# Kernel tuning notes

Hardware: AMD Instinct MI355X
Metric: run time of the kernel (lower is better)

Reference implementation:

```python
import jax, jax.numpy as jnp
import numpy as np

NU, NF, E, FIN, H = 50000, 25000, 500000, 128, 128
NEG_SLOPE_ATT = 0.2   # PyG GATConv default negative_slope
NEG_SLOPE_MLP = 0.01  # nn.LeakyReLU default
BN_EPS = 1e-5


def setup_inputs() -> dict:
    key = jax.random.key(0)
    ks = iter(jax.random.split(key, 64))

    def rn(shape, scale=0.05):
        return jax.random.normal(next(ks), shape, dtype=jnp.float32) * scale

    inp = {
        "x_user": jax.random.normal(next(ks), (NU, FIN), dtype=jnp.float32),
        "x_food": jax.random.normal(next(ks), (NF, FIN), dtype=jnp.float32),
        "uf_src": jax.random.randint(next(ks), (E,), 0, NU),
        "uf_dst": jax.random.randint(next(ks), (E,), 0, NF),
        "fu_src": jax.random.randint(next(ks), (E,), 0, NF),
        "fu_dst": jax.random.randint(next(ks), (E,), 0, NU),
        "he_user": jax.random.randint(next(ks), (E,), 0, NU),
        "he_food": jax.random.randint(next(ks), (E,), 0, NF),
        "batch_health_scores": jax.random.uniform(next(ks), (E,), dtype=jnp.float32),
    }
    # GATConv params per layer (1,2) per edge type (uf: user->food, fu: food->user)
    for L, fin in ((1, FIN), (2, H)):
        for et in ("uf", "fu"):
            inp[f"w{L}_{et}_src"] = rn((fin, H))
            inp[f"w{L}_{et}_dst"] = rn((fin, H))
            inp[f"a{L}_{et}_src"] = rn((H,))
            inp[f"a{L}_{et}_dst"] = rn((H,))
            inp[f"b{L}_{et}"] = jnp.zeros((H,), jnp.float32)
    # BatchNorm per layer per node type
    for L in (1, 2):
        for nt in ("user", "food"):
            inp[f"bn{L}_{nt}_g"] = jnp.ones((H,), jnp.float32)
            inp[f"bn{L}_{nt}_b"] = jnp.zeros((H,), jnp.float32)
    # health preference MLP: Linear(H, H//2) -> LeakyReLU -> Linear(H//2, 1) -> Tanh
    inp["hw1"] = rn((H, H // 2)); inp["hb1"] = jnp.zeros((H // 2,), jnp.float32)
    inp["hw2"] = rn((H // 2, 1)); inp["hb2"] = jnp.zeros((1,), jnp.float32)
    return inp


def _gat(x_src, x_dst, src, dst, w_s, w_d, a_s, a_d, b, n_dst):
    """PyG GATConv, heads=1, no self loops, eval (no attention dropout)."""
    hs = x_src @ w_s                      # [Ns, H]
    hd = x_dst @ w_d                      # [Nd, H]
    asn = hs @ a_s                        # per-src-node scalar
    adn = hd @ a_d                        # per-dst-node scalar
    e = jax.nn.leaky_relu(asn[src] + adn[dst], NEG_SLOPE_ATT)  # [E]
    m = jax.ops.segment_max(e, dst, num_segments=n_dst)
    m = jnp.where(jnp.isfinite(m), m, 0.0)
    ee = jnp.exp(e - m[dst])
    den = jax.ops.segment_sum(ee, dst, num_segments=n_dst)
    alpha = ee / (den[dst] + 1e-16)
    out = jax.ops.segment_sum(alpha[:, None] * hs[src], dst, num_segments=n_dst)
    return out + b


def _bn_elu(x, g, b):
    mu = x.mean(0)
    var = x.var(0)  # biased var, as torch BN uses for normalization
    return jax.nn.elu((x - mu) * jax.lax.rsqrt(var + BN_EPS) * g + b)


def reference(x_user, x_food, uf_src, uf_dst, fu_src, fu_dst, he_user, he_food,
              batch_health_scores,
              w1_uf_src, w1_uf_dst, a1_uf_src, a1_uf_dst, b1_uf,
              w1_fu_src, w1_fu_dst, a1_fu_src, a1_fu_dst, b1_fu,
              w2_uf_src, w2_uf_dst, a2_uf_src, a2_uf_dst, b2_uf,
              w2_fu_src, w2_fu_dst, a2_fu_src, a2_fu_dst, b2_fu,
              bn1_user_g, bn1_user_b, bn1_food_g, bn1_food_b,
              bn2_user_g, bn2_user_b, bn2_food_g, bn2_food_b,
              hw1, hb1, hw2, hb2):
    # ---- layer 1 (HeteroConv, sum aggr; each node type has one incoming edge type)
    xf = _gat(x_user, x_food, uf_src, uf_dst, w1_uf_src, w1_uf_dst, a1_uf_src, a1_uf_dst, b1_uf, NF)
    xu = _gat(x_food, x_user, fu_src, fu_dst, w1_fu_src, w1_fu_dst, a1_fu_src, a1_fu_dst, b1_fu, NU)
    xu = _bn_elu(xu, bn1_user_g, bn1_user_b)
    xf = _bn_elu(xf, bn1_food_g, bn1_food_b)
    # ---- layer 2
    xf2 = _gat(xu, xf, uf_src, uf_dst, w2_uf_src, w2_uf_dst, a2_uf_src, a2_uf_dst, b2_uf, NF)
    xu2 = _gat(xf, xu, fu_src, fu_dst, w2_fu_src, w2_fu_dst, a2_fu_src, a2_fu_dst, b2_fu, NU)
    xu2 = _bn_elu(xu2, bn2_user_g, bn2_user_b)
    xf2 = _bn_elu(xf2, bn2_food_g, bn2_food_b)
    # ---- health-score scatter_add update
    h = jax.nn.leaky_relu(xu2 @ hw1 + hb1, NEG_SLOPE_MLP)
    prefs = jnp.tanh(h @ hw2 + hb2)                      # [NU, 1]
    adjusted = prefs[he_user, 0] * batch_health_scores   # [E]
    # expand+scatter_add over rows == broadcast segment_sum of the per-edge scalar
    s = jax.ops.segment_sum(adjusted, he_food, num_segments=NF)  # [NF]
    xf2 = xf2 + 0.1 * s[:, None]
    return (xu2, xf2, prefs)
```

## Files before the change

kernel.cpp:

```cpp
#include <hip/hip_runtime.h>
#include <cstddef>

#define NU_ 50000
#define NF_ 25000
#define E_  500000
#define CAPF_ 96
#define CAPU_ 48

typedef __attribute__((ext_vector_type(8))) short short8v;
typedef __attribute__((ext_vector_type(4))) float float4v;

constexpr int LDR = 136;

static __device__ __forceinline__ ushort f2bf(float f) {
    uint u = __float_as_uint(f);
    uint r = (u + 0x7fffu + ((u >> 16) & 1u)) >> 16;
    return (ushort)r;
}
static __device__ __forceinline__ float bf2f(ushort u) {
    return __uint_as_float(((uint)u) << 16);
}

struct PPArgs {
    const int* uf_src; const int* uf_dst;
    const int* fu_src; const int* fu_dst;
    int* deg_f; int* deg_u;
    int* buck_f; int* buck_u;
    const float* xu; const float* xf;
    ushort* bu; ushort* bfo;
    const float* W[5];  ushort* T[5];
    const float* waW[8]; const float* waA[8];
    float* vall;
};

__global__ __launch_bounds__(256) void preprocess(PPArgs A) {
    const int EB  = (E_ + 255) / 256;
    const int nbA = NU_ * 32 / 256;
    const int nbB = NF_ * 32 / 256;
    const int nbC = 4 * 64 + 32;
    int b = blockIdx.x, t = threadIdx.x;
    if (b < 2 * EB) {
        const int *src, *dst; int *deg, *buck; int cap, e;
        if (b < EB) { src = A.uf_src; dst = A.uf_dst; deg = A.deg_f; buck = A.buck_f; cap = CAPF_; e = b * 256 + t; }
        else        { src = A.fu_src; dst = A.fu_dst; deg = A.deg_u; buck = A.buck_u; cap = CAPU_; e = (b - EB) * 256 + t; }
        if (e < E_) {
            int d = dst[e];
            int r = atomicAdd(&deg[d], 1);
            if (r < cap) buck[d * cap + r] = src[e];
        }
        return;
    }
    b -= 2 * EB;
    if (b < nbA) {
        int i = b * 256 + t;
        float4 v = ((const float4*)A.xu)[i];
        ushort4 o; o.x = f2bf(v.x); o.y = f2bf(v.y); o.z = f2bf(v.z); o.w = f2bf(v.w);
        ((ushort4*)A.bu)[i] = o;
    } else if (b < nbA + nbB) {
        int i = (b - nbA) * 256 + t;
        float4 v = ((const float4*)A.xf)[i];
        ushort4 o; o.x = f2bf(v.x); o.y = f2bf(v.y); o.z = f2bf(v.z); o.w = f2bf(v.w);
        ((ushort4*)A.bfo)[i] = o;
    } else if (b < nbA + nbB + nbC) {
        int cb = b - nbA - nbB;
        int m, wb, sh;
        if (cb < 256) { m = cb >> 6; wb = cb & 63; sh = 7; }
        else          { m = 4; wb = cb - 256; sh = 6; }
        int idx = wb * 256 + t;
        int k = idx >> sh, c = idx & ((1 << sh) - 1);
        A.T[m][c * 128 + k] = f2bf(A.W[m][idx]);
    } else {
        int db = b - nbA - nbB - nbC;
        int row = db * 4 + (t >> 6);
        int m = row >> 7, k = row & 127, lane = t & 63;
        float2 w = ((const float2*)(A.waW[m] + k * 128))[lane];
        float2 av = ((const float2*)A.waA[m])[lane];
        float s = w.x * av.x + w.y * av.y;
        #pragma unroll
        for (int o = 32; o; o >>= 1) s += __shfl_xor(s, o);
        if (lane == 0) A.vall[row] = s;
    }
}

static __device__ __forceinline__ void gemm_tile(const ushort* __restrict__ Xb,
                                                 const ushort* __restrict__ Wt,
                                                 ushort* __restrict__ C, int N, int row0,
                                                 short* Xs, short* Ws) {
    const int t = threadIdx.x;
    for (int i = t; i < 128 * 16; i += 256) {
        int r = i >> 4, c8 = (i & 15) << 3;
        short8v v = {};
        if (row0 + r < N) v = *(const short8v*)(Xb + (size_t)(row0 + r) * 128 + c8);
        *(short8v*)(&Xs[r * LDR + c8]) = v;
    }
    for (int i = t; i < 128 * 16; i += 256) {
        int r = i >> 4, c8 = (i & 15) << 3;
        *(short8v*)(&Ws[r * LDR + c8]) = *(const short8v*)(Wt + r * 128 + c8);
    }
    __syncthreads();

    const int w = t >> 6, l = t & 63;
    const int m0 = (w & 1) * 64;
    const int n0 = (w >> 1) * 64;
    const int frow = l & 15;
    const int koff = (l >> 4) << 3;

    float4v acc[4][4];
    #pragma unroll
    for (int m = 0; m < 4; ++m)
        #pragma unroll
        for (int n = 0; n < 4; ++n) acc[m][n] = (float4v)0.f;

    #pragma unroll
    for (int ks = 0; ks < 4; ++ks) {
        const int k0 = ks * 32 + koff;
        short8v a[4], b[4];
        #pragma unroll
        for (int m = 0; m < 4; ++m)
            a[m] = *(const short8v*)(&Xs[(m0 + m * 16 + frow) * LDR + k0]);
        #pragma unroll
        for (int n = 0; n < 4; ++n)
            b[n] = *(const short8v*)(&Ws[(n0 + n * 16 + frow) * LDR + k0]);
        #pragma unroll
        for (int m = 0; m < 4; ++m)
            #pragma unroll
            for (int n = 0; n < 4; ++n)
                acc[m][n] = __builtin_amdgcn_mfma_f32_16x16x32_bf16(a[m], b[n], acc[m][n], 0, 0, 0);
    }

    const int crow = (l >> 4) << 2;
    const int ccol = l & 15;
    #pragma unroll
    for (int m = 0; m < 4; ++m) {
        #pragma unroll
        for (int r4 = 0; r4 < 4; ++r4) {
            int grow = row0 + m0 + m * 16 + crow + r4;
            if (grow < N) {
                #pragma unroll
                for (int n = 0; n < 4; ++n)
                    C[(size_t)grow * 128 + n0 + n * 16 + ccol] = f2bf(acc[m][n][r4]);
            }
        }
    }
}

__global__ __launch_bounds__(256) void gemm_both(const ushort* __restrict__ Xu, const ushort* __restrict__ Wtu,
                                                 ushort* __restrict__ Cu,
                                                 const ushort* __restrict__ Xf, const ushort* __restrict__ Wtf,
                                                 ushort* __restrict__ Cf) {
    __shared__ short Xs[128 * LDR];
    __shared__ short Ws[128 * LDR];
    const int GU = (NU_ + 127) / 128;
    if ((int)blockIdx.x < GU)
        gemm_tile(Xu, Wtu, Cu, NU_, blockIdx.x * 128, Xs, Ws);
    else
        gemm_tile(Xf, Wtf, Cf, NF_, (blockIdx.x - GU) * 128, Xs, Ws);
}

__global__ __launch_bounds__(256) void matvec4(const ushort* __restrict__ bu, const ushort* __restrict__ bfo,
                                               const float* __restrict__ v_asn_u, const float* __restrict__ v_adn_u,
                                               const float* __restrict__ v_adn_f, const float* __restrict__ v_asn_f,
                                               float* __restrict__ asn_u, float* __restrict__ adn_u,
                                               float* __restrict__ adn_f, float* __restrict__ asn_f) {
    int row = blockIdx.x * 4 + (threadIdx.x >> 6);
    int lane = threadIdx.x & 63;
    const ushort* X; const float *va, *vb; float *oa, *ob; int r;
    if (row < NU_) { X = bu; va = v_asn_u; vb = v_adn_u; oa = asn_u; ob = adn_u; r = row; }
    else {
        r = row - NU_;
        if (r >= NF_) return;
        X = bfo; va = v_adn_f; vb = v_asn_f; oa = adn_f; ob = asn_f;
    }
    ushort2 x = ((const ushort2*)(X + (size_t)r * 128))[lane];
    float2 va2 = ((const float2*)va)[lane];
    float2 vb2 = ((const float2*)vb)[lane];
    float fx = bf2f(x.x), fy = bf2f(x.y);
    float s1 = fx * va2.x + fy * va2.y;
    float s2 = fx * vb2.x + fy * vb2.y;
    #pragma unroll
    for (int o = 32; o; o >>= 1) { s1 += __shfl_xor(s1, o); s2 += __shfl_xor(s2, o); }
    if (lane == 0) { oa[r] = s1; ob[r] = s2; }
}

__global__ __launch_bounds__(256) void gat_agg_both(
        const int* __restrict__ deg_f, const int* __restrict__ buck_f,
        const float* __restrict__ asn_u, const float* __restrict__ adn_f,
        const ushort* __restrict__ hs_u, ushort* __restrict__ out_f,
        const int* __restrict__ deg_u, const int* __restrict__ buck_u,
        const float* __restrict__ asn_f, const float* __restrict__ adn_u,
        const ushort* __restrict__ hs_f, ushort* __restrict__ out_u) {
    const int NBAF = (NF_ + 3) / 4;
    int blk = blockIdx.x;
    const int *deg, *buck; const float *asn, *adn; const ushort* hs; ushort* out; int Nd, d, cap;
    if (blk < NBAF) {
        deg = deg_f; buck = buck_f; asn = asn_u; adn = adn_f; hs = hs_u; out = out_f;
        Nd = NF_; cap = CAPF_; d = blk * 4 + (threadIdx.x >> 6);
    } else {
        deg = deg_u; buck = buck_u; asn = asn_f; adn = adn_u; hs = hs_f; out = out_u;
        Nd = NU_; cap = CAPU_; d = (blk - NBAF) * 4 + (threadIdx.x >> 6);
    }
    int lane = threadIdx.x & 63;
    if (d >= Nd) return;
    const int beg = d * cap;
    const int end = beg + min(deg[d], cap);
    const float ad = adn[d];
    const int qw = lane >> 4, l16 = lane & 15;
    float acc[8] = {0.f, 0.f, 0.f, 0.f, 0.f, 0.f, 0.f, 0.f};
    float den = 0.f;
    for (int base = beg; base < end; base += 64) {
        int e = base + lane;
        int s = 0; float ev = 0.f;
        if (e < end) {
            s = buck[e];
            float v = asn[s] + ad;
            v = v > 0.f ? v : 0.2f * v;
            ev = __expf(v);
        }
        float r = ev;
        #pragma unroll
        for (int o = 32; o; o >>= 1) r += __shfl_xor(r, o);
        den += r;
        int cnt4 = (min(64, end - base) + 3) & ~3;
        for (int j = 0; j < cnt4; j += 8) {
            int jj = j + qw;
            float ev0 = __shfl(ev, jj);
            int   sj0 = __shfl(s, jj);
            short8v h0 = *(const short8v*)(hs + (size_t)sj0 * 128 + l16 * 8);
            if (j + 4 < cnt4) {
                float ev1 = __shfl(ev, jj + 4);
                int   sj1 = __shfl(s, jj + 4);
                short8v h1 = *(const short8v*)(hs + (size_t)sj1 * 128 + l16 * 8);
                #pragma unroll
                for (int k = 0; k < 8; ++k)
                    acc[k] += ev0 * bf2f((ushort)h0[k]) + ev1 * bf2f((ushort)h1[k]);
            } else {
                #pragma unroll
                for (int k = 0; k < 8; ++k)
                    acc[k] += ev0 * bf2f((ushort)h0[k]);
            }
        }
    }
    #pragma unroll
    for (int k = 0; k < 8; ++k) {
        acc[k] += __shfl_xor(acc[k], 16);
        acc[k] += __shfl_xor(acc[k], 32);
    }
    if (qw == 0) {
        float inv = 1.f / (den + 1e-16f);
        short8v o;
        #pragma unroll
        for (int k = 0; k < 8; ++k) o[k] = (short)f2bf(acc[k] * inv);
        *(short8v*)(out + (size_t)d * 128 + l16 * 8) = o;
    }
}

__global__ __launch_bounds__(256) void bn_stats2b(const ushort* __restrict__ x1, float* __restrict__ stat1,
                                                  int N1, int B1,
                                                  const ushort* __restrict__ x2, float* __restrict__ stat2,
                                                  int N2, int B2) {
    const ushort* x; float* stat; int N, b, nb;
    if ((int)blockIdx.x < B1) { x = x1; stat = stat1; N = N1; b = blockIdx.x; nb = B1; }
    else { x = x2; stat = stat2; N = N2; b = blockIdx.x - B1; nb = B2; }
    const int t = threadIdx.x;
    const int rg = t >> 4;
    const int c16 = t & 15;
    float s[8] = {0,0,0,0,0,0,0,0}, q[8] = {0,0,0,0,0,0,0,0};
    for (int r = b * 16 + rg; r < N; r += nb * 16) {
        short8v v = *(const short8v*)(x + (size_t)r * 128 + c16 * 8);
        #pragma unroll
        for (int k = 0; k < 8; ++k) {
            float f = bf2f((ushort)v[k]);
            s[k] += f; q[k] += f * f;
        }
    }
    #pragma unroll
    for (int k = 0; k < 8; ++k) {
        s[k] += __shfl_xor(s[k], 16); q[k] += __shfl_xor(q[k], 16);
        s[k] += __shfl_xor(s[k], 32); q[k] += __shfl_xor(q[k], 32);
    }
    __shared__ float rs[4][128], rq[4][128];
    const int w = t >> 6, l = t & 63;
    if (l < 16) {
        #pragma unroll
        for (int k = 0; k < 8; ++k) {
            rs[w][l * 8 + k] = s[k];
            rq[w][l * 8 + k] = q[k];
        }
    }
    __syncthreads();
    if (t < 128) {
        atomicAdd(&stat[t],       rs[0][t] + rs[1][t] + rs[2][t] + rs[3][t]);
        atomicAdd(&stat[128 + t], rq[0][t] + rq[1][t] + rq[2][t] + rq[3][t]);
    }
}

__global__ __launch_bounds__(256) void bn_finalize2(float* __restrict__ s1, int N1,
                                                    const float* __restrict__ g1, const float* __restrict__ b1,
                                                    float* __restrict__ s2, int N2,
                                                    const float* __restrict__ g2, const float* __restrict__ b2) {
    int t = threadIdx.x;
    float* s; int N; const float *g, *b; int c;
    if (t < 128) { s = s1; N = N1; g = g1; b = b1; c = t; }
    else         { s = s2; N = N2; g = g2; b = b2; c = t - 128; }
    float invN = 1.0f / N;
    float mu  = s[c] * invN;
    float var = s[128 + c] * invN - mu * mu;
    float sc  = g[c] * rsqrtf(var + 1e-5f);
    s[c]       = sc;
    s[128 + c] = b[c] - mu * sc;
}

__global__ void bn_apply2b(const ushort* __restrict__ x1, const float* __restrict__ ss1,
                           float* __restrict__ xo1, ushort* __restrict__ xb1, int N1,
                           const ushort* __restrict__ x2, const float* __restrict__ ss2,
                           float* __restrict__ xo2, ushort* __restrict__ xb2, int N2) {
    int i = blockIdx.x * 256 + threadIdx.x;
    const ushort* x; const float* ss; float* xo; ushort* xb;
    if (i < N1 * 16) { x = x1; ss = ss1; xo = xo1; xb = xb1; }
    else {
        i -= N1 * 16;
        if (i >= N2 * 16) return;
        x = x2; ss = ss2; xo = xo2; xb = xb2;
    }
    int c16 = i & 15;
    short8v v = *(const short8v*)(x + (size_t)i * 8);
    float sc[8], sh[8];
    *(float4*)&sc[0] = *(const float4*)(ss + c16 * 8);
    *(float4*)&sc[4] = *(const float4*)(ss + c16 * 8 + 4);
    *(float4*)&sh[0] = *(const float4*)(ss + 128 + c16 * 8);
    *(float4*)&sh[4] = *(const float4*)(ss + 128 + c16 * 8 + 4);
    float o[8];
    #pragma unroll
    for (int k = 0; k < 8; ++k) {
        float f = bf2f((ushort)v[k]) * sc[k] + sh[k];
        o[k] = f > 0.f ? f : __expf(f) - 1.f;
    }
    if (xo) {
        *(float4*)(xo + (size_t)i * 8)     = make_float4(o[0], o[1], o[2], o[3]);
        *(float4*)(xo + (size_t)i * 8 + 4) = make_float4(o[4], o[5], o[6], o[7]);
    }
    if (xb) {
        short8v u;
        #pragma unroll
        for (int k = 0; k < 8; ++k) u[k] = (short)f2bf(o[k]);
        *(short8v*)(xb + (size_t)i * 8) = u;
    }
}

__global__ void bn_apply1b(const ushort* __restrict__ x, const float* __restrict__ ss,
                           float* __restrict__ xo, ushort* __restrict__ xb, int N,
                           const float* __restrict__ health) {
    int i = blockIdx.x * 256 + threadIdx.x;
    if (i >= N * 16) return;
    int c16 = i & 15;
    short8v v = *(const short8v*)(x + (size_t)i * 8);
    float sc[8], sh[8];
    *(float4*)&sc[0] = *(const float4*)(ss + c16 * 8);
    *(float4*)&sc[4] = *(const float4*)(ss + c16 * 8 + 4);
    *(float4*)&sh[0] = *(const float4*)(ss + 128 + c16 * 8);
    *(float4*)&sh[4] = *(const float4*)(ss + 128 + c16 * 8 + 4);
    float hv = health ? 0.1f * health[i >> 4] : 0.f;
    float o[8];
    #pragma unroll
    for (int k = 0; k < 8; ++k) {
        float f = bf2f((ushort)v[k]) * sc[k] + sh[k];
        o[k] = (f > 0.f ? f : __expf(f) - 1.f) + hv;
    }
    if (xo) {
        *(float4*)(xo + (size_t)i * 8)     = make_float4(o[0], o[1], o[2], o[3]);
        *(float4*)(xo + (size_t)i * 8 + 4) = make_float4(o[4], o[5], o[6], o[7]);
    }
    if (xb) {
        short8v u;
        #pragma unroll
        for (int k = 0; k < 8; ++k) u[k] = (short)f2bf(o[k]);
        *(short8v*)(xb + (size_t)i * 8) = u;
    }
}

__global__ __launch_bounds__(256) void mlp_mfma(const ushort* __restrict__ Xb,
                                                const ushort* __restrict__ Wt,
                                                const float* __restrict__ hb1,
                                                const float* __restrict__ hw2,
                                                const float* __restrict__ hb2,
                                                float* __restrict__ prefs, int N) {
    __shared__ short Xs[128 * LDR];
    __shared__ short Ws[64 * LDR];
    const int t = threadIdx.x;
    const int row0 = blockIdx.x * 128;

    for (int i = t; i < 128 * 16; i += 256) {
        int r = i >> 4, c8 = (i & 15) << 3;
        short8v v = {};
        if (row0 + r < N) v = *(const short8v*)(Xb + (size_t)(row0 + r) * 128 + c8);
        *(short8v*)(&Xs[r * LDR + c8]) = v;
    }
    for (int i = t; i < 64 * 16; i += 256) {
        int r = i >> 4, c8 = (i & 15) << 3;
        *(short8v*)(&Ws[r * LDR + c8]) = *(const short8v*)(Wt + r * 128 + c8);
    }
    __syncthreads();

    const int w = t >> 6, l = t & 63;
    const int m0 = w * 32;
    const int frow = l & 15;
    const int koff = (l >> 4) << 3;

    float4v acc[2][4];
    #pragma unroll
    for (int m = 0; m < 2; ++m)
        #pragma unroll
        for (int n = 0; n < 4; ++n) acc[m][n] = (float4v)0.f;

    #pragma unroll
    for (int ks = 0; ks < 4; ++ks) {
        const int k0 = ks * 32 + koff;
        short8v a[2], b[4];
        #pragma unroll
        for (int m = 0; m < 2; ++m)
            a[m] = *(const short8v*)(&Xs[(m0 + m * 16 + frow) * LDR + k0]);
        #pragma unroll
        for (int n = 0; n < 4; ++n)
            b[n] = *(const short8v*)(&Ws[(n * 16 + frow) * LDR + k0]);
        #pragma unroll
        for (int m = 0; m < 2; ++m)
            #pragma unroll
            for (int n = 0; n < 4; ++n)
                acc[m][n] = __builtin_amdgcn_mfma_f32_16x16x32_bf16(a[m], b[n], acc[m][n], 0, 0, 0);
    }

    float hb1v[4], hw2v[4];
    #pragma unroll
    for (int n = 0; n < 4; ++n) {
        int col = n * 16 + (l & 15);
        hb1v[n] = hb1[col];
        hw2v[n] = hw2[col];
    }
    const float hb2v = hb2[0];
    #pragma unroll
    for (int m = 0; m < 2; ++m) {
        #pragma unroll
        for (int r4 = 0; r4 < 4; ++r4) {
            float p = 0.f;
            #pragma unroll
            for (int n = 0; n < 4; ++n) {
                float v = acc[m][n][r4] + hb1v[n];
                v = v > 0.f ? v : 0.01f * v;
                p += v * hw2v[n];
            }
            p += __shfl_xor(p, 1);
            p += __shfl_xor(p, 2);
            p += __shfl_xor(p, 4);
            p += __shfl_xor(p, 8);
            int grow = row0 + m0 + m * 16 + ((l >> 4) << 2) + r4;
            if ((l & 15) == 0 && grow < N) prefs[grow] = tanhf(p + hb2v);
        }
    }
}

__global__ void health_scatter(const int* __restrict__ hu, const int* __restrict__ hf,
                               const float* __restrict__ score, const float* __restrict__ prefs,
                               float* __restrict__ s, int E) {
    int e = blockIdx.x * 256 + threadIdx.x;
    if (e >= E) return;
    atomicAdd(&s[hf[e]], prefs[hu[e]] * score[e]);
}

extern "C" void kernel_launch(void* const* d_in, const int* in_sizes, int n_in,
                              void* d_out, int out_size, void* d_ws, size_t ws_size,
                              hipStream_t stream) {
    const float* x_user = (const float*)d_in[0];
    const float* x_food = (const float*)d_in[1];
    const int* uf_src = (const int*)d_in[2];
    const int* uf_dst = (const int*)d_in[3];
    const int* fu_src = (const int*)d_in[4];
    const int* fu_dst = (const int*)d_in[5];
    const int* he_user = (const int*)d_in[6];
    const int* he_food = (const int*)d_in[7];
    const float* scores = (const float*)d_in[8];
    const float* bn1_user_g = (const float*)d_in[29];
    const float* bn1_user_b = (const float*)d_in[30];
    const float* bn1_food_g = (const float*)d_in[31];
    const float* bn1_food_b = (const float*)d_in[32];
    const float* bn2_user_g = (const float*)d_in[33];
    const float* bn2_user_b = (const float*)d_in[34];
    const float* bn2_food_g = (const float*)d_in[35];
    const float* bn2_food_b = (const float*)d_in[36];
    const float* hw1 = (const float*)d_in[37];
    const float* hb1 = (const float*)d_in[38];
    const float* hw2 = (const float*)d_in[39];
    const float* hb2 = (const float*)d_in[40];

    float* outp  = (float*)d_out;
    float* xu2   = outp;
    float* xf2   = outp + (size_t)NU_ * 128;
    float* prefs = xf2 + (size_t)NF_ * 128;

    float* ws = (float*)d_ws;
    ushort* hs_u = (ushort*)ws;
    ushort* hs_f = hs_u + (size_t)NU_ * 128;
    float* base1 = ws + (size_t)(NU_ + NF_) * 64;
    ushort* xu1b = (ushort*)base1;
    ushort* xf1b = xu1b + (size_t)NU_ * 128;
    float* base2 = base1 + (size_t)(NU_ + NF_) * 64;
    ushort* xu2b = (ushort*)base2;
    ushort* xf2b = xu2b + (size_t)NU_ * 128;
    float* base3 = base2 + (size_t)(NU_ + NF_) * 64;
    float* asn_u = base3;
    float* adn_u = asn_u + NU_;
    float* asn_f = adn_u + NU_;
    float* adn_f = asn_f + NF_;
    float* stat4 = adn_f + NF_;
    float* sbuf  = stat4 + 1024;
    int*   deg_f = (int*)(sbuf + NF_);
    int*   deg_u = deg_f + NF_;
    int* buck_f  = deg_u + NU_;
    int* buck_u  = buck_f + (size_t)NF_ * CAPF_;
    ushort* wt0  = (ushort*)(buck_u + (size_t)NU_ * CAPU_);
    ushort* wt1  = wt0 + 16384;
    ushort* wt2  = wt1 + 16384;
    ushort* wt3  = wt2 + 16384;
    ushort* hw1t = wt3 + 16384;
    float* vall  = (float*)(hw1t + 8192);

    const size_t zero_elems = 1024 + NF_ + NF_ + NU_;
    hipMemsetAsync(stat4, 0, zero_elems * sizeof(float), stream);

    const int EB = (E_ + 255) / 256;
    PPArgs pp;
    pp.uf_src = uf_src; pp.uf_dst = uf_dst;
    pp.fu_src = fu_src; pp.fu_dst = fu_dst;
    pp.deg_f = deg_f; pp.deg_u = deg_u;
    pp.buck_f = buck_f; pp.buck_u = buck_u;
    pp.xu = x_user; pp.xf = x_food; pp.bu = xu2b; pp.bfo = xf2b;
    pp.W[0] = (const float*)d_in[9];  pp.T[0] = wt0;
    pp.W[1] = (const float*)d_in[14]; pp.T[1] = wt1;
    pp.W[2] = (const float*)d_in[19]; pp.T[2] = wt2;
    pp.W[3] = (const float*)d_in[24]; pp.T[3] = wt3;
    pp.W[4] = hw1;                    pp.T[4] = hw1t;
    pp.waW[0] = (const float*)d_in[9];  pp.waA[0] = (const float*)d_in[11];
    pp.waW[1] = (const float*)d_in[10]; pp.waA[1] = (const float*)d_in[12];
    pp.waW[2] = (const float*)d_in[14]; pp.waA[2] = (const float*)d_in[16];
    pp.waW[3] = (const float*)d_in[15]; pp.waA[3] = (const float*)d_in[17];
    pp.waW[4] = (const float*)d_in[19]; pp.waA[4] = (const float*)d_in[21];
    pp.waW[5] = (const float*)d_in[20]; pp.waA[5] = (const float*)d_in[22];
    pp.waW[6] = (const float*)d_in[24]; pp.waA[6] = (const float*)d_in[26];
    pp.waW[7] = (const float*)d_in[25]; pp.waA[7] = (const float*)d_in[27];
    pp.vall = vall;
    const int PPB = 2 * EB + NU_ * 32 / 256 + NF_ * 32 / 256 + 288 + 256;
    preprocess<<<PPB, 256, 0, stream>>>(pp);

    const int GB  = (NU_ + 127) / 128 + (NF_ + 127) / 128;
    const int MVB = (NU_ + NF_ + 3) / 4;
    const int AGB = (NF_ + 3) / 4 + (NU_ + 3) / 4;
    const int APB = ((NU_ + NF_) * 16 + 255) / 256;

    gemm_both<<<GB, 256, 0, stream>>>(xu2b, wt0, hs_u, xf2b, wt1, hs_f);
    matvec4<<<MVB, 256, 0, stream>>>(xu2b, xf2b, vall + 0, vall + 384, vall + 128, vall + 256,
                                     asn_u, adn_u, adn_f, asn_f);
    gat_agg_both<<<AGB, 256, 0, stream>>>(deg_f, buck_f, asn_u, adn_f, hs_u, xf1b,
                                          deg_u, buck_u, asn_f, adn_u, hs_f, xu1b);
    bn_stats2b<<<768, 256, 0, stream>>>(xu1b, stat4 + 0, NU_, 512, xf1b, stat4 + 256, NF_, 256);
    bn_finalize2<<<1, 256, 0, stream>>>(stat4 + 0, NU_, bn1_user_g, bn1_user_b,
                                        stat4 + 256, NF_, bn1_food_g, bn1_food_b);
    bn_apply2b<<<APB, 256, 0, stream>>>(xu1b, stat4 + 0,   (float*)nullptr, xu1b, NU_,
                                        xf1b, stat4 + 256, (float*)nullptr, xf1b, NF_);

    gemm_both<<<GB, 256, 0, stream>>>(xu1b, wt2, hs_u, xf1b, wt3, hs_f);
    matvec4<<<MVB, 256, 0, stream>>>(xu1b, xf1b, vall + 512, vall + 896, vall + 640, vall + 768,
                                     asn_u, adn_u, adn_f, asn_f);
    gat_agg_both<<<AGB, 256, 0, stream>>>(deg_f, buck_f, asn_u, adn_f, hs_u, xf2b,
                                          deg_u, buck_u, asn_f, adn_u, hs_f, xu2b);
    bn_stats2b<<<768, 256, 0, stream>>>(xu2b, stat4 + 512, NU_, 512, xf2b, stat4 + 768, NF_, 256);
    bn_finalize2<<<1, 256, 0, stream>>>(stat4 + 512, NU_, bn2_user_g, bn2_user_b,
                                        stat4 + 768, NF_, bn2_food_g, bn2_food_b);
    bn_apply1b<<<(NU_ * 16 + 255) / 256, 256, 0, stream>>>(xu2b, stat4 + 512, xu2, xu2b, NU_,
                                                           (const float*)nullptr);
    mlp_mfma<<<(NU_ + 127) / 128, 256, 0, stream>>>(xu2b, hw1t, hb1, hw2, hb2, prefs, NU_);
    health_scatter<<<EB, 256, 0, stream>>>(he_user, he_food, scores, prefs, sbuf, E_);
    bn_apply1b<<<(NF_ * 16 + 255) / 256, 256, 0, stream>>>(xf2b, stat4 + 768, xf2,
                                                           (ushort*)nullptr, NF_, sbuf);
}
```

Before: 330.2 us.

## Fuse attention matvec into GEMM, fold BN finalize into apply, shrink edge buckets to ushort

The per-node attention projections (asn/adn) are now computed inside the GEMM tile from the X tile already staged in shared memory, which removes the separate matvec4 launches and their re-read of the node features. The BN finalize kernel is dropped, and each apply thread now recomputes scale and shift from the raw sums, gamma, beta and 1/N. Edge bucket source indices are stored as ushort instead of int, halving bucket memory traffic in aggregation. The ushort indices hold only for values below 65536, which fits NU=50000 and NF=25000. The trade-off is extra redundant per-thread BN math and a serial 32-row shuffle reduction added to each GEMM block.

```diff
diff --git a/kernel.cpp b/kernel.cpp
--- a/kernel.cpp
+++ b/kernel.cpp
@@ -25,7 +25,7 @@
     const int* uf_src; const int* uf_dst;
     const int* fu_src; const int* fu_dst;
     int* deg_f; int* deg_u;
-    int* buck_f; int* buck_u;
+    ushort* buck_f; ushort* buck_u;
     const float* xu; const float* xf;
     ushort* bu; ushort* bfo;
     const float* W[5];  ushort* T[5];
@@ -40,13 +40,13 @@
     const int nbC = 4 * 64 + 32;
     int b = blockIdx.x, t = threadIdx.x;
     if (b < 2 * EB) {
-        const int *src, *dst; int *deg, *buck; int cap, e;
+        const int *src, *dst; int *deg; ushort* buck; int cap, e;
         if (b < EB) { src = A.uf_src; dst = A.uf_dst; deg = A.deg_f; buck = A.buck_f; cap = CAPF_; e = b * 256 + t; }
         else        { src = A.fu_src; dst = A.fu_dst; deg = A.deg_u; buck = A.buck_u; cap = CAPU_; e = (b - EB) * 256 + t; }
         if (e < E_) {
             int d = dst[e];
             int r = atomicAdd(&deg[d], 1);
-            if (r < cap) buck[d * cap + r] = src[e];
+            if (r < cap) buck[d * cap + r] = (ushort)src[e];
         }
         return;
     }
@@ -85,6 +85,8 @@
 static __device__ __forceinline__ void gemm_tile(const ushort* __restrict__ Xb,
                                                  const ushort* __restrict__ Wt,
                                                  ushort* __restrict__ C, int N, int row0,
+                                                 const float* __restrict__ va, const float* __restrict__ vb,
+                                                 float* __restrict__ oa, float* __restrict__ ob,
                                                  short* Xs, short* Ws) {
     const int t = threadIdx.x;
     for (int i = t; i < 128 * 16; i += 256) {
@@ -142,56 +144,48 @@
             }
         }
     }
-}
-
-__global__ __launch_bounds__(256) void gemm_both(const ushort* __restrict__ Xu, const ushort* __restrict__ Wtu,
-                                                 ushort* __restrict__ Cu,
-                                                 const ushort* __restrict__ Xf, const ushort* __restrict__ Wtf,
-                                                 ushort* __restrict__ Cf) {
+
+    float2 va2 = ((const float2*)va)[l];
+    float2 vb2 = ((const float2*)vb)[l];
+    for (int rr = 0; rr < 32; ++rr) {
+        int r = w * 32 + rr;
+        ushort2 xv = *(const ushort2*)(&Xs[r * LDR + l * 2]);
+        float fx = bf2f(xv.x), fy = bf2f(xv.y);
+        float s1 = fx * va2.x + fy * va2.y;
+        float s2 = fx * vb2.x + fy * vb2.y;
+        #pragma unroll
+        for (int o = 32; o; o >>= 1) { s1 += __shfl_xor(s1, o); s2 += __shfl_xor(s2, o); }
+        int grow = row0 + r;
+        if (l == 0 && grow < N) { oa[grow] = s1; ob[grow] = s2; }
+    }
+}
+
+__global__ __launch_bounds__(256) void gemm_both(
+        const ushort* __restrict__ Xu, const ushort* __restrict__ Wtu, ushort* __restrict__ Cu,
+        const float* __restrict__ vau, const float* __restrict__ vbu,
+        float* __restrict__ oau, float* __restrict__ obu,
+        const ushort* __restrict__ Xf, const ushort* __restrict__ Wtf, ushort* __restrict__ Cf,
+        const float* __restrict__ vaf, const float* __restrict__ vbf,
+        float* __restrict__ oaf, float* __restrict__ obf) {
     __shared__ short Xs[128 * LDR];
     __shared__ short Ws[128 * LDR];
     const int GU = (NU_ + 127) / 128;
     if ((int)blockIdx.x < GU)
-        gemm_tile(Xu, Wtu, Cu, NU_, blockIdx.x * 128, Xs, Ws);
+        gemm_tile(Xu, Wtu, Cu, NU_, blockIdx.x * 128, vau, vbu, oau, obu, Xs, Ws);
     else
-        gemm_tile(Xf, Wtf, Cf, NF_, (blockIdx.x - GU) * 128, Xs, Ws);
-}
-
-__global__ __launch_bounds__(256) void matvec4(const ushort* __restrict__ bu, const ushort* __restrict__ bfo,
-                                               const float* __restrict__ v_asn_u, const float* __restrict__ v_adn_u,
-                                               const float* __restrict__ v_adn_f, const float* __restrict__ v_asn_f,
-                                               float* __restrict__ asn_u, float* __restrict__ adn_u,
-                                               float* __restrict__ adn_f, float* __restrict__ asn_f) {
-    int row = blockIdx.x * 4 + (threadIdx.x >> 6);
-    int lane = threadIdx.x & 63;
-    const ushort* X; const float *va, *vb; float *oa, *ob; int r;
-    if (row < NU_) { X = bu; va = v_asn_u; vb = v_adn_u; oa = asn_u; ob = adn_u; r = row; }
-    else {
-        r = row - NU_;
-        if (r >= NF_) return;
-        X = bfo; va = v_adn_f; vb = v_asn_f; oa = adn_f; ob = asn_f;
-    }
-    ushort2 x = ((const ushort2*)(X + (size_t)r * 128))[lane];
-    float2 va2 = ((const float2*)va)[lane];
-    float2 vb2 = ((const float2*)vb)[lane];
-    float fx = bf2f(x.x), fy = bf2f(x.y);
-    float s1 = fx * va2.x + fy * va2.y;
-    float s2 = fx * vb2.x + fy * vb2.y;
-    #pragma unroll
-    for (int o = 32; o; o >>= 1) { s1 += __shfl_xor(s1, o); s2 += __shfl_xor(s2, o); }
-    if (lane == 0) { oa[r] = s1; ob[r] = s2; }
+        gemm_tile(Xf, Wtf, Cf, NF_, (blockIdx.x - GU) * 128, vaf, vbf, oaf, obf, Xs, Ws);
 }
 
 __global__ __launch_bounds__(256) void gat_agg_both(
-        const int* __restrict__ deg_f, const int* __restrict__ buck_f,
+        const int* __restrict__ deg_f, const ushort* __restrict__ buck_f,
         const float* __restrict__ asn_u, const float* __restrict__ adn_f,
         const ushort* __restrict__ hs_u, ushort* __restrict__ out_f,
-        const int* __restrict__ deg_u, const int* __restrict__ buck_u,
+        const int* __restrict__ deg_u, const ushort* __restrict__ buck_u,
         const float* __restrict__ asn_f, const float* __restrict__ adn_u,
         const ushort* __restrict__ hs_f, ushort* __restrict__ out_u) {
     const int NBAF = (NF_ + 3) / 4;
     int blk = blockIdx.x;
-    const int *deg, *buck; const float *asn, *adn; const ushort* hs; ushort* out; int Nd, d, cap;
+    const int* deg; const ushort* buck; const float *asn, *adn; const ushort* hs; ushort* out; int Nd, d, cap;
     if (blk < NBAF) {
         deg = deg_f; buck = buck_f; asn = asn_u; adn = adn_f; hs = hs_u; out = out_f;
         Nd = NF_; cap = CAPF_; d = blk * 4 + (threadIdx.x >> 6);
@@ -294,41 +288,40 @@
     }
 }
 
-__global__ __launch_bounds__(256) void bn_finalize2(float* __restrict__ s1, int N1,
-                                                    const float* __restrict__ g1, const float* __restrict__ b1,
-                                                    float* __restrict__ s2, int N2,
-                                                    const float* __restrict__ g2, const float* __restrict__ b2) {
-    int t = threadIdx.x;
-    float* s; int N; const float *g, *b; int c;
-    if (t < 128) { s = s1; N = N1; g = g1; b = b1; c = t; }
-    else         { s = s2; N = N2; g = g2; b = b2; c = t - 128; }
-    float invN = 1.0f / N;
-    float mu  = s[c] * invN;
-    float var = s[128 + c] * invN - mu * mu;
-    float sc  = g[c] * rsqrtf(var + 1e-5f);
-    s[c]       = sc;
-    s[128 + c] = b[c] - mu * sc;
-}
-
-__global__ void bn_apply2b(const ushort* __restrict__ x1, const float* __restrict__ ss1,
+static __device__ __forceinline__ void bn_scale_shift(const float* __restrict__ stat,
+                                                      const float* __restrict__ g,
+                                                      const float* __restrict__ b,
+                                                      float invN, int c0,
+                                                      float* sc, float* sh) {
+    #pragma unroll
+    for (int k = 0; k < 8; ++k) {
+        int c = c0 + k;
+        float mu  = stat[c] * invN;
+        float var = stat[128 + c] * invN - mu * mu;
+        float s = g[c] * rsqrtf(var + 1e-5f);
+        sc[k] = s;
+        sh[k] = b[c] - mu * s;
+    }
+}
+
+__global__ void bn_apply2b(const ushort* __restrict__ x1, const float* __restrict__ stat1,
+                           const float* __restrict__ g1, const float* __restrict__ b1, float invN1,
                            float* __restrict__ xo1, ushort* __restrict__ xb1, int N1,
-                           const ushort* __restrict__ x2, const float* __restrict__ ss2,
+                           const ushort* __restrict__ x2, const float* __restrict__ stat2,
+                           const float* __restrict__ g2, const float* __restrict__ b2, float invN2,
                            float* __restrict__ xo2, ushort* __restrict__ xb2, int N2) {
     int i = blockIdx.x * 256 + threadIdx.x;
-    const ushort* x; const float* ss; float* xo; ushort* xb;
-    if (i < N1 * 16) { x = x1; ss = ss1; xo = xo1; xb = xb1; }
+    const ushort* x; const float *stat, *g, *b; float invN; float* xo; ushort* xb;
+    if (i < N1 * 16) { x = x1; stat = stat1; g = g1; b = b1; invN = invN1; xo = xo1; xb = xb1; }
     else {
         i -= N1 * 16;
         if (i >= N2 * 16) return;
-        x = x2; ss = ss2; xo = xo2; xb = xb2;
+        x = x2; stat = stat2; g = g2; b = b2; invN = invN2; xo = xo2; xb = xb2;
     }
     int c16 = i & 15;
     short8v v = *(const short8v*)(x + (size_t)i * 8);
     float sc[8], sh[8];
-    *(float4*)&sc[0] = *(const float4*)(ss + c16 * 8);
-    *(float4*)&sc[4] = *(const float4*)(ss + c16 * 8 + 4);
-    *(float4*)&sh[0] = *(const float4*)(ss + 128 + c16 * 8);
-    *(float4*)&sh[4] = *(const float4*)(ss + 128 + c16 * 8 + 4);
+    bn_scale_shift(stat, g, b, invN, c16 * 8, sc, sh);
     float o[8];
     #pragma unroll
     for (int k = 0; k < 8; ++k) {
@@ -347,7 +340,8 @@
     }
 }
 
-__global__ void bn_apply1b(const ushort* __restrict__ x, const float* __restrict__ ss,
+__global__ void bn_apply1b(const ushort* __restrict__ x, const float* __restrict__ stat,
+                           const float* __restrict__ g, const float* __restrict__ b, float invN,
                            float* __restrict__ xo, ushort* __restrict__ xb, int N,
                            const float* __restrict__ health) {
     int i = blockIdx.x * 256 + threadIdx.x;
@@ -355,10 +349,7 @@
     int c16 = i & 15;
     short8v v = *(const short8v*)(x + (size_t)i * 8);
     float sc[8], sh[8];
-    *(float4*)&sc[0] = *(const float4*)(ss + c16 * 8);
-    *(float4*)&sc[4] = *(const float4*)(ss + c16 * 8 + 4);
-    *(float4*)&sh[0] = *(const float4*)(ss + 128 + c16 * 8);
-    *(float4*)&sh[4] = *(const float4*)(ss + 128 + c16 * 8 + 4);
+    bn_scale_shift(stat, g, b, invN, c16 * 8, sc, sh);
     float hv = health ? 0.1f * health[i >> 4] : 0.f;
     float o[8];
     #pragma unroll
@@ -514,9 +505,9 @@
     float* sbuf  = stat4 + 1024;
     int*   deg_f = (int*)(sbuf + NF_);
     int*   deg_u = deg_f + NF_;
-    int* buck_f  = deg_u + NU_;
-    int* buck_u  = buck_f + (size_t)NF_ * CAPF_;
-    ushort* wt0  = (ushort*)(buck_u + (size_t)NU_ * CAPU_);
+    ushort* buck_f = (ushort*)(deg_u + NU_);
+    ushort* buck_u = buck_f + (size_t)NF_ * CAPF_;
+    ushort* wt0  = buck_u + (size_t)NU_ * CAPU_;
     ushort* wt1  = wt0 + 16384;
     ushort* wt2  = wt1 + 16384;
     ushort* wt3  = wt2 + 16384;
@@ -551,33 +542,30 @@
     preprocess<<<PPB, 256, 0, stream>>>(pp);
 
     const int GB  = (NU_ + 127) / 128 + (NF_ + 127) / 128;
-    const int MVB = (NU_ + NF_ + 3) / 4;
     const int AGB = (NF_ + 3) / 4 + (NU_ + 3) / 4;
     const int APB = ((NU_ + NF_) * 16 + 255) / 256;
-
-    gemm_both<<<GB, 256, 0, stream>>>(xu2b, wt0, hs_u, xf2b, wt1, hs_f);
-    matvec4<<<MVB, 256, 0, stream>>>(xu2b, xf2b, vall + 0, vall + 384, vall + 128, vall + 256,
-                                     asn_u, adn_u, adn_f, asn_f);
+    const float invNU = 1.0f / NU_, invNF = 1.0f / NF_;
+
+    gemm_both<<<GB, 256, 0, stream>>>(
+        xu2b, wt0, hs_u, vall + 0,   vall + 384, asn_u, adn_u,
+        xf2b, wt1, hs_f, vall + 256, vall + 128, asn_f, adn_f);
     gat_agg_both<<<AGB, 256, 0, stream>>>(deg_f, buck_f, asn_u, adn_f, hs_u, xf1b,
                                           deg_u, buck_u, asn_f, adn_u, hs_f, xu1b);
     bn_stats2b<<<768, 256, 0, stream>>>(xu1b, stat4 + 0, NU_, 512, xf1b, stat4 + 256, NF_, 256);
-    bn_finalize2<<<1, 256, 0, stream>>>(stat4 + 0, NU_, bn1_user_g, bn1_user_b,
-                                        stat4 + 256, NF_, bn1_food_g, bn1_food_b);
-    bn_apply2b<<<APB, 256, 0, stream>>>(xu1b, stat4 + 0,   (float*)nullptr, xu1b, NU_,
-                                        xf1b, stat4 + 256, (float*)nullptr, xf1b, NF_);
-
-    gemm_both<<<GB, 256, 0, stream>>>(xu1b, wt2, hs_u, xf1b, wt3, hs_f);
-    matvec4<<<MVB, 256, 0, stream>>>(xu1b, xf1b, vall + 512, vall + 896, vall + 640, vall + 768,
-                                     asn_u, adn_u, adn_f, asn_f);
+    bn_apply2b<<<APB, 256, 0, stream>>>(
+        xu1b, stat4 + 0,   bn1_user_g, bn1_user_b, invNU, (float*)nullptr, xu1b, NU_,
+        xf1b, stat4 + 256, bn1_food_g, bn1_food_b, invNF, (float*)nullptr, xf1b, NF_);
+
+    gemm_both<<<GB, 256, 0, stream>>>(
+        xu1b, wt2, hs_u, vall + 512, vall + 896, asn_u, adn_u,
+        xf1b, wt3, hs_f, vall + 768, vall + 640, asn_f, adn_f);
     gat_agg_both<<<AGB, 256, 0, stream>>>(deg_f, buck_f, asn_u, adn_f, hs_u, xf2b,
                                           deg_u, buck_u, asn_f, adn_u, hs_f, xu2b);
     bn_stats2b<<<768, 256, 0, stream>>>(xu2b, stat4 + 512, NU_, 512, xf2b, stat4 + 768, NF_, 256);
-    bn_finalize2<<<1, 256, 0, stream>>>(stat4 + 512, NU_, bn2_user_g, bn2_user_b,
-                                        stat4 + 768, NF_, bn2_food_g, bn2_food_b);
-    bn_apply1b<<<(NU_ * 16 + 255) / 256, 256, 0, stream>>>(xu2b, stat4 + 512, xu2, xu2b, NU_,
-                                                           (const float*)nullptr);
+    bn_apply1b<<<(NU_ * 16 + 255) / 256, 256, 0, stream>>>(
+        xu2b, stat4 + 512, bn2_user_g, bn2_user_b, invNU, xu2, xu2b, NU_, (const float*)nullptr);
     mlp_mfma<<<(NU_ + 127) / 128, 256, 0, stream>>>(xu2b, hw1t, hb1, hw2, hb2, prefs, NU_);
     health_scatter<<<EB, 256, 0, stream>>>(he_user, he_food, scores, prefs, sbuf, E_);
-    bn_apply1b<<<(NF_ * 16 + 255) / 256, 256, 0, stream>>>(xf2b, stat4 + 768, xf2,
-                                                           (ushort*)nullptr, NF_, sbuf);
-}
+    bn_apply1b<<<(NF_ * 16 + 255) / 256, 256, 0, stream>>>(
+        xf2b, stat4 + 768, bn2_food_g, bn2_food_b, invNF, xf2, (ushort*)nullptr, NF_, sbuf);
+}
```

Result: no change. 336.5 us (+1.9%).
